# Performance work log

Measured on AMD Instinct MI355X. Metric: run time of the kernel, lower is better.

Reference implementation:

```python
import jax, jax.numpy as jnp
from jax import lax
import numpy as np

B = 8192
NUM_CTX = 300; NUM_STN = 300; NUM_GPE = 20; NUM_GPI = 2; NUM_OUT = 20
FF_DIM = 20; FF_STEPS = 20; STN_ITERS = 50
ETA_GPE = 1.0; ETA_STN = 1.0 / 3.0; ETA_GPI = 0.1
A1 = 1.0; A2 = 1.0; THETAD1 = 0.0; THETAD2 = 0.0
UNITS = (64, 128, 64)

_SPECS = [("vf0", UNITS[0], NUM_CTX), ("vf1", UNITS[1], UNITS[0]), ("vf2", UNITS[2], UNITS[1]), ("vf3", 1, UNITS[2]),
          ("jd1", FF_DIM, NUM_CTX), ("jd2", FF_DIM, NUM_CTX), ("kd1", FF_DIM, NUM_CTX), ("kd2", FF_DIM, NUM_CTX),
          ("sg", NUM_GPE, NUM_STN), ("gs", NUM_STN, NUM_GPE), ("glat", NUM_GPE, NUM_GPE), ("slat", NUM_STN, NUM_STN),
          ("d1gpi", NUM_GPI, FF_DIM), ("stngpi", NUM_GPI, NUM_STN),
          ("ih", 4 * NUM_OUT, NUM_GPI), ("hh", 4 * NUM_OUT, NUM_OUT)]


def _lin_init(k, out_d, in_d):
    kw, kb = jax.random.split(k)
    bound = 1.0 / np.sqrt(in_d)
    w = jax.random.uniform(kw, (out_d, in_d), minval=-bound, maxval=bound, dtype=jnp.float32)
    b = jax.random.uniform(kb, (out_d,), minval=-bound, maxval=bound, dtype=jnp.float32)
    return w, b


def setup_inputs() -> dict:
    key = jax.random.key(0)
    ks = iter(jax.random.split(key, 40))
    inp = {}
    inp["stimulus"] = jax.random.normal(next(ks), (B, NUM_CTX), dtype=jnp.float32)
    inp["deltavf"] = jax.random.normal(next(ks), (B, 1), dtype=jnp.float32)
    inp["hx0"] = jax.random.uniform(next(ks), (B, NUM_OUT), dtype=jnp.float32)
    inp["cx0"] = jax.random.uniform(next(ks), (B, NUM_OUT), dtype=jnp.float32)
    for name, o, i in _SPECS:
        w, b = _lin_init(next(ks), o, i)
        inp["w_" + name] = w
        inp["b_" + name] = b
    return inp


def _lin(x, w, b):
    return x @ w.T + b


def _lstm_cell(x, h, c, w_ih, b_ih, w_hh, b_hh):
    gates = _lin(x, w_ih, b_ih) + _lin(h, w_hh, b_hh)
    i, f, g, o = jnp.split(gates, 4, axis=-1)  # torch LSTMCell gate order
    c_new = jax.nn.sigmoid(f) * c + jax.nn.sigmoid(i) * jnp.tanh(g)
    h_new = jax.nn.sigmoid(o) * jnp.tanh(c_new)
    return h_new, c_new


def reference(stimulus, deltavf, hx0, cx0,
              w_vf0, b_vf0, w_vf1, b_vf1, w_vf2, b_vf2, w_vf3, b_vf3,
              w_jd1, b_jd1, w_jd2, b_jd2, w_kd1, b_kd1, w_kd2, b_kd2,
              w_sg, b_sg, w_gs, b_gs, w_glat, b_glat, w_slat, b_slat,
              w_d1gpi, b_d1gpi, w_stngpi, b_stngpi,
              w_ih, b_ih, w_hh, b_hh):
    bsz = stimulus.shape[0]
    # value function head
    h = jax.nn.relu(_lin(stimulus, w_vf0, b_vf0))
    h = jax.nn.relu(_lin(h, w_vf1, b_vf1))
    h = jax.nn.relu(_lin(h, w_vf2, b_vf2))
    vt = jnp.tanh(_lin(h, w_vf3, b_vf3))  # [B, 1]

    lamd1 = jax.nn.sigmoid(A1 * (deltavf - THETAD1))  # [B, 1]
    lamd2 = jax.nn.sigmoid(A2 * (deltavf - THETAD2))  # [B, 1]

    # loop-invariant striatal drives (computed every iter in torch, same value)
    J_D1 = _lin(stimulus, w_jd1, b_jd1)
    J_D2 = _lin(stimulus, w_jd2, b_jd2)
    K_D1 = _lin(stimulus, w_kd1, b_kd1)
    K_D2 = _lin(stimulus, w_kd2, b_kd2)

    def ff_step(carry, _):
        v1, v2 = carry
        v1 = jax.nn.sigmoid(lamd1 * (J_D1 * (1.0 - v1) + (1.0 - K_D1) * v1))
        v2 = jax.nn.sigmoid(lamd2 * (J_D2 * (1.0 - v2) + (1.0 - K_D2) * v2))
        return (v1, v2), None

    z_ff = jnp.zeros((bsz, FF_DIM), dtype=stimulus.dtype)
    (V_D1, V_D2), _ = lax.scan(ff_step, (z_ff, z_ff), None, length=FF_STEPS)

    V_GPi_DP = _lin(V_D1, w_d1gpi, b_d1gpi)  # [B, num_gpi]

    def stn_step(carry, _):
        xgpe, xstn, vstn, vgpi, hx, cx = carry
        xgpe = xgpe + ETA_GPE * (-xgpe + _lin(vstn, w_sg, b_sg) + _lin(xgpe, w_glat, b_glat) - V_D2)
        xstn = xstn + ETA_STN * (-xstn + _lin(xgpe, w_gs, b_gs) + _lin(vstn, w_slat, b_slat))
        vstn = jnp.tanh(lamd2 * xstn)
        V_GPi_IP = lamd2 * _lin(vstn, w_stngpi, b_stngpi)
        vgpi = vgpi + ETA_GPI * (-vgpi - V_GPi_DP + 2.0 * V_GPi_IP)
        hx, cx = _lstm_cell(-vgpi, hx, cx, w_ih, b_ih, w_hh, b_hh)
        return (xgpe, xstn, vstn, vgpi, hx, cx), None

    carry0 = (jnp.zeros((bsz, NUM_GPE), dtype=stimulus.dtype),
              jnp.zeros((bsz, NUM_STN), dtype=stimulus.dtype),
              jnp.zeros((bsz, NUM_STN), dtype=stimulus.dtype),  # tanh(lamd2*0) = 0
              jnp.zeros((bsz, NUM_GPI), dtype=stimulus.dtype),
              hx0, cx0)
    carry, _ = lax.scan(stn_step, carry0, None, length=STN_ITERS)
    hx = carry[4]
    return hx, vt
```

## Files before the change

kernel.cpp:

```cpp
#include <hip/hip_runtime.h>


typedef _Float16 f16_t;
typedef _Float16 f16x8 __attribute__((ext_vector_type(8)));
typedef _Float16 f16x4 __attribute__((ext_vector_type(4)));
typedef float floatx4 __attribute__((ext_vector_type(4)));
typedef float floatx2 __attribute__((ext_vector_type(2)));

#define BTOT 8192
#define BM   32
#define NTHR 512
#define NBLK 256
#define VSTR 328
#define XST  32

struct Params {
  const float *stimulus, *deltavf, *hx0, *cx0;
  const float *w_vf0, *b_vf0, *w_vf1, *b_vf1, *w_vf2, *b_vf2, *w_vf3, *b_vf3;
  const float *w_jd1, *b_jd1, *w_jd2, *b_jd2, *w_kd1, *b_kd1, *w_kd2, *b_kd2;
  const float *w_sg, *b_sg, *w_gs, *b_gs, *w_glat, *b_glat, *w_slat, *b_slat;
  const float *w_d1gpi, *b_d1gpi, *w_stngpi, *b_stngpi;
  const float *w_ih, *b_ih, *w_hh, *b_hh;
  float* out;
};

struct __align__(16) Smem {
  f16_t vstn[BM * VSTR];
  f16_t xgpe[2][BM * XST];
  f16_t hxf[BM * XST];
  f16_t wB2[21 * 512];
  f16_t wsp[10 * 512];
  f16_t whh[5 * 512];
  union { float h1f[BM * 128]; float scr[3200]; float gates[BM * 80]; } u;
  float h0f[BM * 64];
  float V_D2f[BM * 20];
  float lstmc[20][12];
  float bsumS[304];
  float bsg[20];
  float DPs[BM * 2], vgpis[BM * 2], lamS[BM];
};

__device__ __forceinline__ float rcp_f(float x) { return __builtin_amdgcn_rcpf(x); }
__device__ __forceinline__ float sigm_fast(float x) { return rcp_f(1.f + __expf(-x)); }
__device__ __forceinline__ float tanh_fast(float x) { return 1.f - 2.f * rcp_f(1.f + __expf(2.f * x)); }

__device__ __forceinline__ f16x8 ldfrag(const float* row, int k0, int kmax, bool valid) {
  float4 z = make_float4(0.f, 0.f, 0.f, 0.f);
  int nv = valid ? (kmax - k0) : 0;
  float4 f0 = (nv >= 4) ? *(const float4*)(row + k0) : z;
  float4 f1 = (nv >= 8) ? *(const float4*)(row + k0 + 4) : z;
  f16x8 r;
  r[0] = (f16_t)f0.x; r[1] = (f16_t)f0.y; r[2] = (f16_t)f0.z; r[3] = (f16_t)f0.w;
  r[4] = (f16_t)f1.x; r[5] = (f16_t)f1.y; r[6] = (f16_t)f1.z; r[7] = (f16_t)f1.w;
  return r;
}

__global__ __launch_bounds__(NTHR, 2) void bg_main(Params P) {
  __shared__ Smem S;
  const int tid  = threadIdx.x;
  const int lane = tid & 63;
  const int wv   = tid >> 6;
  const int q    = lane >> 4;
  const int cl   = lane & 15;
  const int row0 = blockIdx.x * BM;
  const floatx4 zf = {0.f, 0.f, 0.f, 0.f};

  if (tid < BM) S.lamS[tid] = sigm_fast(P.deltavf[row0 + tid]);
  for (int i = tid; i < BM * 2; i += NTHR) S.vgpis[i] = 0.f;
  for (int i = tid; i < 2 * BM * XST; i += NTHR) ((f16_t*)S.xgpe)[i] = (f16_t)0.f;
  for (int i = tid; i < BM * XST; i += NTHR) {
    int m = i >> 5, j = i & 31;
    S.hxf[i] = (j < 20) ? (f16_t)P.hx0[row0 * 20 + m * 20 + j] : (f16_t)0.f;
  }
  for (int i = tid; i < BM * VSTR; i += NTHR) S.vstn[i] = (f16_t)0.f;
  for (int i = tid; i < 21 * 512; i += NTHR) {
    int t = i >> 9, l = (i >> 3) & 63, jj = i & 7;
    int c2 = l & 15, k = ((l >> 4) << 3) + jj;
    float v = 0.f;
    if (t < 19) { int n = t * 16 + c2; if (n < 300 && k < 20) v = P.w_gs[n * 20 + k]; }
    else        { int g = (t - 19) * 16 + c2; if (g < 20 && k < 20) v = P.w_glat[g * 20 + k]; }
    S.wB2[i] = (f16_t)v;
  }
  for (int i = tid; i < 10 * 512; i += NTHR) {
    int c = i >> 9, l = (i >> 3) & 63, jj = i & 7;
    int p = l & 15, k = c * 32 + ((l >> 4) << 3) + jj;
    float v = (p < 2 && k < 300) ? P.w_stngpi[p * 300 + k] : 0.f;
    S.wsp[i] = (f16_t)v;
  }
  for (int i = tid; i < 5 * 512; i += NTHR) {
    int t = i >> 9, l = (i >> 3) & 63, jj = i & 7;
    int c2 = l & 15, k = ((l >> 4) << 3) + jj;
    int orig = (c2 & 3) * 20 + 4 * t + (c2 >> 2);
    S.whh[i] = (f16_t)((k < 20) ? P.w_hh[orig * 20 + k] : 0.f);
  }
  for (int i = tid; i < 240; i += NTHR) {
    int j = i / 12, c = i - j * 12;
    float v;
    if (c < 4)      v = P.b_ih[c * 20 + j] + P.b_hh[c * 20 + j];
    else if (c < 8) v = P.w_ih[((c - 4) * 20 + j) * 2 + 0];
    else            v = P.w_ih[((c - 8) * 20 + j) * 2 + 1];
    S.lstmc[j][c] = v;
  }
  for (int i = tid; i < 304; i += NTHR) S.bsumS[i] = (i < 300) ? (P.b_slat[i] + P.b_gs[i]) : 0.f;
  for (int i = tid; i < 20; i += NTHR)  S.bsg[i] = P.b_sg[i] + P.b_glat[i];

  {
    int o = tid & 63, mb = (tid >> 6) * 4;
    const float4* wr = (const float4*)(P.w_vf0 + o * 300);
    float bias = P.b_vf0[o], a[4];
#pragma unroll
    for (int u = 0; u < 4; ++u) a[u] = bias;
    for (int kq = 0; kq < 75; ++kq) {
      float4 w = wr[kq];
#pragma unroll
      for (int u = 0; u < 4; ++u) {
        float4 v = *(const float4*)(P.stimulus + (size_t)(row0 + mb + u) * 300 + kq * 4);
        a[u] = fmaf(v.x, w.x, a[u]); a[u] = fmaf(v.y, w.y, a[u]);
        a[u] = fmaf(v.z, w.z, a[u]); a[u] = fmaf(v.w, w.w, a[u]);
      }
    }
#pragma unroll
    for (int u = 0; u < 4; ++u) S.h0f[(mb + u) * 64 + o] = fmaxf(a[u], 0.f);
  }
  __syncthreads();
  {
    int o = tid & 127, mb = (tid >> 7) * 8;
    const float* wr = P.w_vf1 + o * 64;
    float bias = P.b_vf1[o], a[8];
#pragma unroll
    for (int u = 0; u < 8; ++u) a[u] = bias;
    for (int k = 0; k < 64; ++k) {
      float w = wr[k];
#pragma unroll
      for (int u = 0; u < 8; ++u) a[u] = fmaf(S.h0f[(mb + u) * 64 + k], w, a[u]);
    }
#pragma unroll
    for (int u = 0; u < 8; ++u) S.u.h1f[(mb + u) * 128 + o] = fmaxf(a[u], 0.f);
  }
  __syncthreads();
  {
    int o = tid & 63, mb = (tid >> 6) * 4;
    const float* wr = P.w_vf2 + o * 128;
    float bias = P.b_vf2[o], a[4];
#pragma unroll
    for (int u = 0; u < 4; ++u) a[u] = bias;
    for (int k = 0; k < 128; ++k) {
      float w = wr[k];
#pragma unroll
      for (int u = 0; u < 4; ++u) a[u] = fmaf(S.u.h1f[(mb + u) * 128 + k], w, a[u]);
    }
#pragma unroll
    for (int u = 0; u < 4; ++u) S.h0f[(mb + u) * 64 + o] = fmaxf(a[u], 0.f);
  }
  __syncthreads();
  {
    int oid = tid & 127, mb = (tid >> 7) * 8;
    if (oid < 80) {
      int which = oid / 20, o = oid - which * 20;
      const float *wp, *bp;
      if (which == 0)      { wp = P.w_jd1; bp = P.b_jd1; }
      else if (which == 1) { wp = P.w_jd2; bp = P.b_jd2; }
      else if (which == 2) { wp = P.w_kd1; bp = P.b_kd1; }
      else                 { wp = P.w_kd2; bp = P.b_kd2; }
      float bias = bp[o], a[8];
#pragma unroll
      for (int u = 0; u < 8; ++u) a[u] = bias;
      for (int kq = 0; kq < 75; ++kq) {
        float4 w = *(const float4*)(wp + o * 300 + kq * 4);
#pragma unroll
        for (int u = 0; u < 8; ++u) {
          float4 v = *(const float4*)(P.stimulus + (size_t)(row0 + mb + u) * 300 + kq * 4);
          a[u] = fmaf(v.x, w.x, a[u]); a[u] = fmaf(v.y, w.y, a[u]);
          a[u] = fmaf(v.z, w.z, a[u]); a[u] = fmaf(v.w, w.w, a[u]);
        }
      }
#pragma unroll
      for (int u = 0; u < 8; ++u) S.u.scr[which * 640 + (mb + u) * 20 + o] = a[u];
    }
    if (tid < BM) {
      float a = P.b_vf3[0];
      for (int k = 0; k < 64; ++k) a = fmaf(S.h0f[tid * 64 + k], P.w_vf3[k], a);
      P.out[(size_t)BTOT * 20 + row0 + tid] = tanh_fast(a);
    }
  }
  __syncthreads();
  for (int i = tid; i < BM * 20; i += NTHR) {
    int m = i / 20;
    float j1 = S.u.scr[i],        j2 = S.u.scr[640 + i];
    float k1 = S.u.scr[1280 + i], k2 = S.u.scr[1920 + i];
    float L = S.lamS[m], v1 = 0.f, v2 = 0.f;
    for (int s = 0; s < 20; ++s) {
      v1 = sigm_fast(L * (j1 * (1.f - v1) + (1.f - k1) * v1));
      v2 = sigm_fast(L * (j2 * (1.f - v2) + (1.f - k2) * v2));
    }
    S.u.scr[2560 + i] = v1;
    S.V_D2f[i] = v2;
  }
  __syncthreads();
  if (tid < BM * 2) {
    int m = tid >> 1, p2 = tid & 1;
    float a = P.b_d1gpi[p2];
    for (int o = 0; o < 20; ++o) a = fmaf(S.u.scr[2560 + m * 20 + o], P.w_d1gpi[p2 * 20 + o], a);
    S.DPs[tid] = a;
  }
  __syncthreads();

  f16x8 Ws[3][10];
#pragma unroll
  for (int j = 0; j < 3; ++j) {
    int t = wv + 8 * j;
    if (t < 19) {
      int n = t * 16 + cl;
#pragma unroll
      for (int c = 0; c < 10; ++c)
        Ws[j][c] = ldfrag(P.w_slat + (size_t)(n < 300 ? n : 0) * 300, c * 32 + q * 8, 300, n < 300);
    } else if (t < 21) {
      int g = (t - 19) * 16 + cl;
#pragma unroll
      for (int c = 0; c < 10; ++c)
        Ws[j][c] = ldfrag(P.w_sg + (size_t)(g < 20 ? g : 0) * 300, c * 32 + q * 8, 300, g < 20);
    } else {
      f16x8 z;
#pragma unroll
      for (int e = 0; e < 8; ++e) z[e] = (f16_t)0.f;
#pragma unroll
      for (int c = 0; c < 10; ++c) Ws[j][c] = z;
    }
  }
  const float lam0 = S.lamS[cl], lam1 = S.lamS[cl + 16];
  const float bstn0 = P.b_stngpi[0], bstn1 = P.b_stngpi[1];
  const int e0 = tid,        m0 = e0 / 20, j0 = e0 - m0 * 20;
  const int e1 = tid + NTHR, m1 = e1 / 20, j1 = e1 - m1 * 20;
  const bool hase1 = (tid < BM * 20 - NTHR);
  float cxr0 = P.cx0[row0 * 20 + e0], hxr0 = P.hx0[row0 * 20 + e0];
  float cxr1 = hase1 ? P.cx0[row0 * 20 + e1] : 0.f;
  float hxr1 = hase1 ? P.hx0[row0 * 20 + e1] : 0.f;
  const bool isSgW = (wv == 3 || wv == 4);

  floatx4 acc[3][2];
#pragma unroll
  for (int j = 0; j < 3; ++j) { acc[j][0] = zf; acc[j][1] = zf; }

  for (int it = 0; it < 50; ++it) {
    const int po = it & 1, pn = po ^ 1;
    if (isSgW) { acc[2][0] = zf; acc[2][1] = zf; }

    __builtin_amdgcn_s_setprio(1);
#pragma unroll
    for (int c = 0; c < 10; ++c) {
      f16x8 b0 = *(const f16x8*)&S.vstn[cl * VSTR + c * 32 + q * 8];
      f16x8 b1 = *(const f16x8*)&S.vstn[(16 + cl) * VSTR + c * 32 + q * 8];
#pragma unroll
      for (int j = 0; j < 3; ++j) {
        if (wv + 8 * j < 21) {
          acc[j][0] = __builtin_amdgcn_mfma_f32_16x16x32_f16(Ws[j][c], b0, acc[j][0], 0, 0, 0);
          acc[j][1] = __builtin_amdgcn_mfma_f32_16x16x32_f16(Ws[j][c], b1, acc[j][1], 0, 0, 0);
        }
      }
    }
    __builtin_amdgcn_s_setprio(0);
    if (isSgW) {
      f16x8 Wg = *(const f16x8*)&S.wB2[(wv + 16) * 512 + lane * 8];
      f16x8 g0 = *(const f16x8*)&S.xgpe[po][cl * XST + q * 8];
      f16x8 g1 = *(const f16x8*)&S.xgpe[po][(16 + cl) * XST + q * 8];
      acc[2][0] = __builtin_amdgcn_mfma_f32_16x16x32_f16(Wg, g0, acc[2][0], 0, 0, 0);
      acc[2][1] = __builtin_amdgcn_mfma_f32_16x16x32_f16(Wg, g1, acc[2][1], 0, 0, 0);
      int g0i = (wv - 3) * 16 + q * 4;
      if (g0i < 20) {
        floatx4 bg4 = *(const floatx4*)&S.bsg[g0i];
#pragma unroll
        for (int mf = 0; mf < 2; ++mf) {
          int batch = cl + 16 * mf;
          floatx4 vd4 = *(const floatx4*)&S.V_D2f[batch * 20 + g0i];
          f16x4 pk;
#pragma unroll
          for (int r = 0; r < 4; ++r) pk[r] = (f16_t)(acc[2][mf][r] + bg4[r] - vd4[r]);
          *(f16x4*)&S.xgpe[pn][batch * XST + g0i] = pk;
        }
      }
    }
    __syncthreads();

    {
      f16x8 x0 = *(const f16x8*)&S.xgpe[pn][cl * XST + q * 8];
      f16x8 x1 = *(const f16x8*)&S.xgpe[pn][(16 + cl) * XST + q * 8];
      if (wv < 5) {
        f16x8 Wh = *(const f16x8*)&S.whh[wv * 512 + lane * 8];
        f16x8 h0 = *(const f16x8*)&S.hxf[cl * XST + q * 8];
        f16x8 h1 = *(const f16x8*)&S.hxf[(16 + cl) * XST + q * 8];
        floatx4 gA = __builtin_amdgcn_mfma_f32_16x16x32_f16(Wh, h0, zf, 0, 0, 0);
        floatx4 gB = __builtin_amdgcn_mfma_f32_16x16x32_f16(Wh, h1, zf, 0, 0, 0);
        int gb = wv * 16 + q * 4;
        *(floatx4*)&S.u.gates[cl * 80 + gb] = gA;
        *(floatx4*)&S.u.gates[(cl + 16) * 80 + gb] = gB;
      }
#pragma unroll
      for (int j = 0; j < 3; ++j) {
        int t = wv + 8 * j;
        if (t < 19) {
          f16x8 Wg = *(const f16x8*)&S.wB2[t * 512 + lane * 8];
          acc[j][0] = __builtin_amdgcn_mfma_f32_16x16x32_f16(Wg, x0, acc[j][0], 0, 0, 0);
          acc[j][1] = __builtin_amdgcn_mfma_f32_16x16x32_f16(Wg, x1, acc[j][1], 0, 0, 0);
        }
      }
#pragma unroll
      for (int j = 0; j < 3; ++j) {
        int t = wv + 8 * j;
        if (t < 19) {
          int n0 = t * 16 + q * 4;
          if (!(t == 18 && q == 3)) {
            floatx4 bs4 = *(const floatx4*)&S.bsumS[n0];
#pragma unroll
            for (int mf = 0; mf < 2; ++mf) {
              float lm = mf ? lam1 : lam0;
              f16x4 pk;
#pragma unroll
              for (int r = 0; r < 4; ++r) {
                float tmp = acc[j][mf][r] + bs4[r];
                float xn  = tmp * (1.0f / 3.0f);
                acc[j][mf][r] = tmp * (2.0f / 3.0f);
                pk[r] = (f16_t)tanh_fast(lm * xn);
              }
              *(f16x4*)&S.vstn[(cl + 16 * mf) * VSTR + n0] = pk;
            }
          }
        }
      }
    }
    __syncthreads();

    if (wv == 5) {
      floatx4 ip0 = zf, ip1 = zf;
#pragma unroll
      for (int c = 0; c < 10; ++c) {
        f16x8 Wp = *(const f16x8*)&S.wsp[c * 512 + lane * 8];
        f16x8 b0 = *(const f16x8*)&S.vstn[cl * VSTR + c * 32 + q * 8];
        f16x8 b1 = *(const f16x8*)&S.vstn[(16 + cl) * VSTR + c * 32 + q * 8];
        ip0 = __builtin_amdgcn_mfma_f32_16x16x32_f16(Wp, b0, ip0, 0, 0, 0);
        ip1 = __builtin_amdgcn_mfma_f32_16x16x32_f16(Wp, b1, ip1, 0, 0, 0);
      }
      if (q == 0) {
#pragma unroll
        for (int mf = 0; mf < 2; ++mf) {
          int batch = cl + 16 * mf;
          float lm = mf ? lam1 : lam0;
          floatx2 vg = *(const floatx2*)&S.vgpis[batch * 2];
          floatx2 dp = *(const floatx2*)&S.DPs[batch * 2];
          float ipa = lm * ((mf ? ip1[0] : ip0[0]) + bstn0);
          float ipb = lm * ((mf ? ip1[1] : ip0[1]) + bstn1);
          vg[0] = vg[0] + 0.1f * (-vg[0] - dp[0] + 2.f * ipa);
          vg[1] = vg[1] + 0.1f * (-vg[1] - dp[1] + 2.f * ipb);
          *(floatx2*)&S.vgpis[batch * 2] = vg;
        }
      }
    }
    __syncthreads();

    {
      floatx4 g4 = *(const floatx4*)&S.u.gates[m0 * 80 + j0 * 4];
      floatx4 cb = *(const floatx4*)&S.lstmc[j0][0];
      floatx4 w0 = *(const floatx4*)&S.lstmc[j0][4];
      floatx4 w1 = *(const floatx4*)&S.lstmc[j0][8];
      floatx2 vg = *(const floatx2*)&S.vgpis[m0 * 2];
      float gi = g4[0] + cb[0] - w0[0] * vg[0] - w1[0] * vg[1];
      float gf = g4[1] + cb[1] - w0[1] * vg[0] - w1[1] * vg[1];
      float gg = g4[2] + cb[2] - w0[2] * vg[0] - w1[2] * vg[1];
      float go = g4[3] + cb[3] - w0[3] * vg[0] - w1[3] * vg[1];
      float cn = sigm_fast(gf) * cxr0 + sigm_fast(gi) * tanh_fast(gg);
      cxr0 = cn;
      hxr0 = sigm_fast(go) * tanh_fast(cn);
      S.hxf[m0 * XST + j0] = (f16_t)hxr0;
    }
    if (hase1) {
      floatx4 g4 = *(const floatx4*)&S.u.gates[m1 * 80 + j1 * 4];
      floatx4 cb = *(const floatx4*)&S.lstmc[j1][0];
      floatx4 w0 = *(const floatx4*)&S.lstmc[j1][4];
      floatx4 w1 = *(const floatx4*)&S.lstmc[j1][8];
      floatx2 vg = *(const floatx2*)&S.vgpis[m1 * 2];
      float gi = g4[0] + cb[0] - w0[0] * vg[0] - w1[0] * vg[1];
      float gf = g4[1] + cb[1] - w0[1] * vg[0] - w1[1] * vg[1];
      float gg = g4[2] + cb[2] - w0[2] * vg[0] - w1[2] * vg[1];
      float go = g4[3] + cb[3] - w0[3] * vg[0] - w1[3] * vg[1];
      float cn = sigm_fast(gf) * cxr1 + sigm_fast(gi) * tanh_fast(gg);
      cxr1 = cn;
      hxr1 = sigm_fast(go) * tanh_fast(cn);
      S.hxf[m1 * XST + j1] = (f16_t)hxr1;
    }
  }

  P.out[(size_t)row0 * 20 + e0] = hxr0;
  if (hase1) P.out[(size_t)row0 * 20 + e1] = hxr1;
}

extern "C" void kernel_launch(void* const* d_in, const int* in_sizes, int n_in,
                              void* d_out, int out_size, void* d_ws, size_t ws_size,
                              hipStream_t stream) {
  (void)in_sizes; (void)n_in; (void)out_size; (void)d_ws; (void)ws_size;
  Params P;
  P.stimulus = (const float*)d_in[0];
  P.deltavf  = (const float*)d_in[1];
  P.hx0 = (const float*)d_in[2];
  P.cx0 = (const float*)d_in[3];
  P.w_vf0 = (const float*)d_in[4];  P.b_vf0 = (const float*)d_in[5];
  P.w_vf1 = (const float*)d_in[6];  P.b_vf1 = (const float*)d_in[7];
  P.w_vf2 = (const float*)d_in[8];  P.b_vf2 = (const float*)d_in[9];
  P.w_vf3 = (const float*)d_in[10]; P.b_vf3 = (const float*)d_in[11];
  P.w_jd1 = (const float*)d_in[12]; P.b_jd1 = (const float*)d_in[13];
  P.w_jd2 = (const float*)d_in[14]; P.b_jd2 = (const float*)d_in[15];
  P.w_kd1 = (const float*)d_in[16]; P.b_kd1 = (const float*)d_in[17];
  P.w_kd2 = (const float*)d_in[18]; P.b_kd2 = (const float*)d_in[19];
  P.w_sg  = (const float*)d_in[20]; P.b_sg  = (const float*)d_in[21];
  P.w_gs  = (const float*)d_in[22]; P.b_gs  = (const float*)d_in[23];
  P.w_glat= (const float*)d_in[24]; P.b_glat= (const float*)d_in[25];
  P.w_slat= (const float*)d_in[26]; P.b_slat= (const float*)d_in[27];
  P.w_d1gpi  = (const float*)d_in[28]; P.b_d1gpi  = (const float*)d_in[29];
  P.w_stngpi = (const float*)d_in[30]; P.b_stngpi = (const float*)d_in[31];
  P.w_ih = (const float*)d_in[32]; P.b_ih = (const float*)d_in[33];
  P.w_hh = (const float*)d_in[34]; P.b_hh = (const float*)d_in[35];
  P.out  = (float*)d_out;
  bg_main<<<NBLK, NTHR, 0, stream>>>(P);
}
```

Before: 408.2 us.

## Double threads per block and redistribute STN recurrence tiles across sixteen waves

Raises the block to 1024 threads with one block per CU and redistributes the 21 MFMA output tiles of the STN/GPe recurrence so each of 16 waves owns at most two tiles. The second tile's weights now come from a new shared-memory staging buffer instead of registers. The LSTM gate MFMAs, the GPi reduction and the elementwise LSTM update move to otherwise idle waves, so the update runs in one pass per element. The aim is shorter per-iteration critical paths and lower register pressure, at the cost of more LDS, lower block occupancy and extra LDS reads each iteration.

```diff
diff --git a/kernel.cpp b/kernel.cpp
--- a/kernel.cpp
+++ b/kernel.cpp
@@ -9,7 +9,7 @@
 
 #define BTOT 8192
 #define BM   32
-#define NTHR 512
+#define NTHR 1024
 #define NBLK 256
 #define VSTR 328
 #define XST  32
@@ -29,6 +29,7 @@
   f16_t xgpe[2][BM * XST];
   f16_t hxf[BM * XST];
   f16_t wB2[21 * 512];
+  f16_t ws1[5 * 10 * 512];
   f16_t wsp[10 * 512];
   f16_t whh[5 * 512];
   union { float h1f[BM * 128]; float scr[3200]; float gates[BM * 80]; } u;
@@ -55,7 +56,7 @@
   return r;
 }
 
-__global__ __launch_bounds__(NTHR, 2) void bg_main(Params P) {
+__global__ __launch_bounds__(NTHR, 1) void bg_main(Params P) {
   __shared__ Smem S;
   const int tid  = threadIdx.x;
   const int lane = tid & 63;
@@ -65,12 +66,16 @@
   const int row0 = blockIdx.x * BM;
   const floatx4 zf = {0.f, 0.f, 0.f, 0.f};
 
+  const bool has1  = (wv < 5);
+  const bool isSgW = (wv == 3 || wv == 4);
+  const int  gtile = (wv >= 5 && wv < 10) ? (wv - 5) : -1;
+
   if (tid < BM) S.lamS[tid] = sigm_fast(P.deltavf[row0 + tid]);
   for (int i = tid; i < BM * 2; i += NTHR) S.vgpis[i] = 0.f;
   for (int i = tid; i < 2 * BM * XST; i += NTHR) ((f16_t*)S.xgpe)[i] = (f16_t)0.f;
   for (int i = tid; i < BM * XST; i += NTHR) {
     int m = i >> 5, j = i & 31;
-    S.hxf[i] = (j < 20) ? (f16_t)P.hx0[row0 * 20 + m * 20 + j] : (f16_t)0.f;
+    S.hxf[i] = (j < 20) ? (f16_t)P.hx0[(size_t)(row0 + m) * 20 + j] : (f16_t)0.f;
   }
   for (int i = tid; i < BM * VSTR; i += NTHR) S.vstn[i] = (f16_t)0.f;
   for (int i = tid; i < 21 * 512; i += NTHR) {
@@ -81,6 +86,16 @@
     else        { int g = (t - 19) * 16 + c2; if (g < 20 && k < 20) v = P.w_glat[g * 20 + k]; }
     S.wB2[i] = (f16_t)v;
   }
+  for (int i = tid; i < 5 * 5120; i += NTHR) {
+    int t5 = i / 5120, rem = i - t5 * 5120;
+    int c = rem >> 9, l = (rem >> 3) & 63, jj = i & 7;
+    int c2 = l & 15, k = c * 32 + ((l >> 4) << 3) + jj;
+    int t = 16 + t5;
+    float v = 0.f;
+    if (t < 19) { int n = t * 16 + c2; if (n < 300 && k < 300) v = P.w_slat[(size_t)n * 300 + k]; }
+    else        { int g = (t - 19) * 16 + c2; if (g < 20 && k < 300) v = P.w_sg[(size_t)g * 300 + k]; }
+    S.ws1[i] = (f16_t)v;
+  }
   for (int i = tid; i < 10 * 512; i += NTHR) {
     int c = i >> 9, l = (i >> 3) & 63, jj = i & 7;
     int p = l & 15, k = c * 32 + ((l >> 4) << 3) + jj;
@@ -105,56 +120,54 @@
   for (int i = tid; i < 20; i += NTHR)  S.bsg[i] = P.b_sg[i] + P.b_glat[i];
 
   {
-    int o = tid & 63, mb = (tid >> 6) * 4;
+    int o = tid & 63, mb = (tid >> 6) * 2;
     const float4* wr = (const float4*)(P.w_vf0 + o * 300);
-    float bias = P.b_vf0[o], a[4];
-#pragma unroll
-    for (int u = 0; u < 4; ++u) a[u] = bias;
+    float bias = P.b_vf0[o], a[2];
+    a[0] = bias; a[1] = bias;
     for (int kq = 0; kq < 75; ++kq) {
       float4 w = wr[kq];
 #pragma unroll
-      for (int u = 0; u < 4; ++u) {
+      for (int u = 0; u < 2; ++u) {
         float4 v = *(const float4*)(P.stimulus + (size_t)(row0 + mb + u) * 300 + kq * 4);
         a[u] = fmaf(v.x, w.x, a[u]); a[u] = fmaf(v.y, w.y, a[u]);
         a[u] = fmaf(v.z, w.z, a[u]); a[u] = fmaf(v.w, w.w, a[u]);
       }
     }
 #pragma unroll
-    for (int u = 0; u < 4; ++u) S.h0f[(mb + u) * 64 + o] = fmaxf(a[u], 0.f);
+    for (int u = 0; u < 2; ++u) S.h0f[(mb + u) * 64 + o] = fmaxf(a[u], 0.f);
   }
   __syncthreads();
   {
-    int o = tid & 127, mb = (tid >> 7) * 8;
+    int o = tid & 127, mb = (tid >> 7) * 4;
     const float* wr = P.w_vf1 + o * 64;
-    float bias = P.b_vf1[o], a[8];
-#pragma unroll
-    for (int u = 0; u < 8; ++u) a[u] = bias;
+    float bias = P.b_vf1[o], a[4];
+#pragma unroll
+    for (int u = 0; u < 4; ++u) a[u] = bias;
     for (int k = 0; k < 64; ++k) {
       float w = wr[k];
 #pragma unroll
-      for (int u = 0; u < 8; ++u) a[u] = fmaf(S.h0f[(mb + u) * 64 + k], w, a[u]);
-    }
-#pragma unroll
-    for (int u = 0; u < 8; ++u) S.u.h1f[(mb + u) * 128 + o] = fmaxf(a[u], 0.f);
+      for (int u = 0; u < 4; ++u) a[u] = fmaf(S.h0f[(mb + u) * 64 + k], w, a[u]);
+    }
+#pragma unroll
+    for (int u = 0; u < 4; ++u) S.u.h1f[(mb + u) * 128 + o] = fmaxf(a[u], 0.f);
   }
   __syncthreads();
   {
-    int o = tid & 63, mb = (tid >> 6) * 4;
+    int o = tid & 63, mb = (tid >> 6) * 2;
     const float* wr = P.w_vf2 + o * 128;
-    float bias = P.b_vf2[o], a[4];
-#pragma unroll
-    for (int u = 0; u < 4; ++u) a[u] = bias;
+    float bias = P.b_vf2[o], a[2];
+    a[0] = bias; a[1] = bias;
     for (int k = 0; k < 128; ++k) {
       float w = wr[k];
 #pragma unroll
-      for (int u = 0; u < 4; ++u) a[u] = fmaf(S.u.h1f[(mb + u) * 128 + k], w, a[u]);
-    }
-#pragma unroll
-    for (int u = 0; u < 4; ++u) S.h0f[(mb + u) * 64 + o] = fmaxf(a[u], 0.f);
+      for (int u = 0; u < 2; ++u) a[u] = fmaf(S.u.h1f[(mb + u) * 128 + k], w, a[u]);
+    }
+#pragma unroll
+    for (int u = 0; u < 2; ++u) S.h0f[(mb + u) * 64 + o] = fmaxf(a[u], 0.f);
   }
   __syncthreads();
   {
-    int oid = tid & 127, mb = (tid >> 7) * 8;
+    int oid = tid & 127, mb = (tid >> 7) * 4;
     if (oid < 80) {
       int which = oid / 20, o = oid - which * 20;
       const float *wp, *bp;
@@ -162,20 +175,20 @@
       else if (which == 1) { wp = P.w_jd2; bp = P.b_jd2; }
       else if (which == 2) { wp = P.w_kd1; bp = P.b_kd1; }
       else                 { wp = P.w_kd2; bp = P.b_kd2; }
-      float bias = bp[o], a[8];
-#pragma unroll
-      for (int u = 0; u < 8; ++u) a[u] = bias;
+      float bias = bp[o], a[4];
+#pragma unroll
+      for (int u = 0; u < 4; ++u) a[u] = bias;
       for (int kq = 0; kq < 75; ++kq) {
         float4 w = *(const float4*)(wp + o * 300 + kq * 4);
 #pragma unroll
-        for (int u = 0; u < 8; ++u) {
+        for (int u = 0; u < 4; ++u) {
           float4 v = *(const float4*)(P.stimulus + (size_t)(row0 + mb + u) * 300 + kq * 4);
           a[u] = fmaf(v.x, w.x, a[u]); a[u] = fmaf(v.y, w.y, a[u]);
           a[u] = fmaf(v.z, w.z, a[u]); a[u] = fmaf(v.w, w.w, a[u]);
         }
       }
 #pragma unroll
-      for (int u = 0; u < 8; ++u) S.u.scr[which * 640 + (mb + u) * 20 + o] = a[u];
+      for (int u = 0; u < 4; ++u) S.u.scr[which * 640 + (mb + u) * 20 + o] = a[u];
     }
     if (tid < BM) {
       float a = P.b_vf3[0];
@@ -205,66 +218,56 @@
   }
   __syncthreads();
 
-  f16x8 Ws[3][10];
-#pragma unroll
-  for (int j = 0; j < 3; ++j) {
-    int t = wv + 8 * j;
-    if (t < 19) {
-      int n = t * 16 + cl;
-#pragma unroll
-      for (int c = 0; c < 10; ++c)
-        Ws[j][c] = ldfrag(P.w_slat + (size_t)(n < 300 ? n : 0) * 300, c * 32 + q * 8, 300, n < 300);
-    } else if (t < 21) {
-      int g = (t - 19) * 16 + cl;
-#pragma unroll
-      for (int c = 0; c < 10; ++c)
-        Ws[j][c] = ldfrag(P.w_sg + (size_t)(g < 20 ? g : 0) * 300, c * 32 + q * 8, 300, g < 20);
-    } else {
-      f16x8 z;
-#pragma unroll
-      for (int e = 0; e < 8; ++e) z[e] = (f16_t)0.f;
-#pragma unroll
-      for (int c = 0; c < 10; ++c) Ws[j][c] = z;
-    }
+  f16x8 Ws0[10];
+  {
+    int n = wv * 16 + cl;
+    const float* a0 = P.w_slat + (size_t)n * 300;
+#pragma unroll
+    for (int c = 0; c < 10; ++c) Ws0[c] = ldfrag(a0, c * 32 + q * 8, 300, true);
   }
   const float lam0 = S.lamS[cl], lam1 = S.lamS[cl + 16];
   const float bstn0 = P.b_stngpi[0], bstn1 = P.b_stngpi[1];
-  const int e0 = tid,        m0 = e0 / 20, j0 = e0 - m0 * 20;
-  const int e1 = tid + NTHR, m1 = e1 / 20, j1 = e1 - m1 * 20;
-  const bool hase1 = (tid < BM * 20 - NTHR);
-  float cxr0 = P.cx0[row0 * 20 + e0], hxr0 = P.hx0[row0 * 20 + e0];
-  float cxr1 = hase1 ? P.cx0[row0 * 20 + e1] : 0.f;
-  float hxr1 = hase1 ? P.hx0[row0 * 20 + e1] : 0.f;
-  const bool isSgW = (wv == 3 || wv == 4);
-
-  floatx4 acc[3][2];
-#pragma unroll
-  for (int j = 0; j < 3; ++j) { acc[j][0] = zf; acc[j][1] = zf; }
+  const bool lown = (tid >= 384);
+  const int  e0 = lown ? (tid - 384) : 0;
+  const int  m0 = e0 / 20, j0 = e0 - m0 * 20;
+  float cxr0 = lown ? P.cx0[(size_t)row0 * 20 + e0] : 0.f;
+  float hxr0 = 0.f;
+
+  floatx4 acc[2][2];
+  acc[0][0] = zf; acc[0][1] = zf; acc[1][0] = zf; acc[1][1] = zf;
 
   for (int it = 0; it < 50; ++it) {
     const int po = it & 1, pn = po ^ 1;
-    if (isSgW) { acc[2][0] = zf; acc[2][1] = zf; }
+    if (isSgW) { acc[1][0] = zf; acc[1][1] = zf; }
 
     __builtin_amdgcn_s_setprio(1);
-#pragma unroll
-    for (int c = 0; c < 10; ++c) {
-      f16x8 b0 = *(const f16x8*)&S.vstn[cl * VSTR + c * 32 + q * 8];
-      f16x8 b1 = *(const f16x8*)&S.vstn[(16 + cl) * VSTR + c * 32 + q * 8];
-#pragma unroll
-      for (int j = 0; j < 3; ++j) {
-        if (wv + 8 * j < 21) {
-          acc[j][0] = __builtin_amdgcn_mfma_f32_16x16x32_f16(Ws[j][c], b0, acc[j][0], 0, 0, 0);
-          acc[j][1] = __builtin_amdgcn_mfma_f32_16x16x32_f16(Ws[j][c], b1, acc[j][1], 0, 0, 0);
-        }
+    if (has1) {
+#pragma unroll
+      for (int c = 0; c < 10; ++c) {
+        f16x8 b0 = *(const f16x8*)&S.vstn[cl * VSTR + c * 32 + q * 8];
+        f16x8 b1 = *(const f16x8*)&S.vstn[(16 + cl) * VSTR + c * 32 + q * 8];
+        f16x8 a1 = *(const f16x8*)&S.ws1[(wv * 10 + c) * 512 + lane * 8];
+        acc[0][0] = __builtin_amdgcn_mfma_f32_16x16x32_f16(Ws0[c], b0, acc[0][0], 0, 0, 0);
+        acc[0][1] = __builtin_amdgcn_mfma_f32_16x16x32_f16(Ws0[c], b1, acc[0][1], 0, 0, 0);
+        acc[1][0] = __builtin_amdgcn_mfma_f32_16x16x32_f16(a1, b0, acc[1][0], 0, 0, 0);
+        acc[1][1] = __builtin_amdgcn_mfma_f32_16x16x32_f16(a1, b1, acc[1][1], 0, 0, 0);
+      }
+    } else {
+#pragma unroll
+      for (int c = 0; c < 10; ++c) {
+        f16x8 b0 = *(const f16x8*)&S.vstn[cl * VSTR + c * 32 + q * 8];
+        f16x8 b1 = *(const f16x8*)&S.vstn[(16 + cl) * VSTR + c * 32 + q * 8];
+        acc[0][0] = __builtin_amdgcn_mfma_f32_16x16x32_f16(Ws0[c], b0, acc[0][0], 0, 0, 0);
+        acc[0][1] = __builtin_amdgcn_mfma_f32_16x16x32_f16(Ws0[c], b1, acc[0][1], 0, 0, 0);
       }
     }
     __builtin_amdgcn_s_setprio(0);
     if (isSgW) {
-      f16x8 Wg = *(const f16x8*)&S.wB2[(wv + 16) * 512 + lane * 8];
+      f16x8 Wg = *(const f16x8*)&S.wB2[(16 + wv) * 512 + lane * 8];
       f16x8 g0 = *(const f16x8*)&S.xgpe[po][cl * XST + q * 8];
       f16x8 g1 = *(const f16x8*)&S.xgpe[po][(16 + cl) * XST + q * 8];
-      acc[2][0] = __builtin_amdgcn_mfma_f32_16x16x32_f16(Wg, g0, acc[2][0], 0, 0, 0);
-      acc[2][1] = __builtin_amdgcn_mfma_f32_16x16x32_f16(Wg, g1, acc[2][1], 0, 0, 0);
+      acc[1][0] = __builtin_amdgcn_mfma_f32_16x16x32_f16(Wg, g0, acc[1][0], 0, 0, 0);
+      acc[1][1] = __builtin_amdgcn_mfma_f32_16x16x32_f16(Wg, g1, acc[1][1], 0, 0, 0);
       int g0i = (wv - 3) * 16 + q * 4;
       if (g0i < 20) {
         floatx4 bg4 = *(const floatx4*)&S.bsg[g0i];
@@ -274,7 +277,7 @@
           floatx4 vd4 = *(const floatx4*)&S.V_D2f[batch * 20 + g0i];
           f16x4 pk;
 #pragma unroll
-          for (int r = 0; r < 4; ++r) pk[r] = (f16_t)(acc[2][mf][r] + bg4[r] - vd4[r]);
+          for (int r = 0; r < 4; ++r) pk[r] = (f16_t)(acc[1][mf][r] + bg4[r] - vd4[r]);
           *(f16x4*)&S.xgpe[pn][batch * XST + g0i] = pk;
         }
       }
@@ -284,19 +287,19 @@
     {
       f16x8 x0 = *(const f16x8*)&S.xgpe[pn][cl * XST + q * 8];
       f16x8 x1 = *(const f16x8*)&S.xgpe[pn][(16 + cl) * XST + q * 8];
-      if (wv < 5) {
-        f16x8 Wh = *(const f16x8*)&S.whh[wv * 512 + lane * 8];
+      if (gtile >= 0) {
+        f16x8 Wh = *(const f16x8*)&S.whh[gtile * 512 + lane * 8];
         f16x8 h0 = *(const f16x8*)&S.hxf[cl * XST + q * 8];
         f16x8 h1 = *(const f16x8*)&S.hxf[(16 + cl) * XST + q * 8];
         floatx4 gA = __builtin_amdgcn_mfma_f32_16x16x32_f16(Wh, h0, zf, 0, 0, 0);
         floatx4 gB = __builtin_amdgcn_mfma_f32_16x16x32_f16(Wh, h1, zf, 0, 0, 0);
-        int gb = wv * 16 + q * 4;
+        int gb = gtile * 16 + q * 4;
         *(floatx4*)&S.u.gates[cl * 80 + gb] = gA;
         *(floatx4*)&S.u.gates[(cl + 16) * 80 + gb] = gB;
       }
 #pragma unroll
-      for (int j = 0; j < 3; ++j) {
-        int t = wv + 8 * j;
+      for (int j = 0; j < 2; ++j) {
+        int t = j ? (has1 ? 16 + wv : 99) : wv;
         if (t < 19) {
           f16x8 Wg = *(const f16x8*)&S.wB2[t * 512 + lane * 8];
           acc[j][0] = __builtin_amdgcn_mfma_f32_16x16x32_f16(Wg, x0, acc[j][0], 0, 0, 0);
@@ -304,8 +307,8 @@
         }
       }
 #pragma unroll
-      for (int j = 0; j < 3; ++j) {
-        int t = wv + 8 * j;
+      for (int j = 0; j < 2; ++j) {
+        int t = j ? (has1 ? 16 + wv : 99) : wv;
         if (t < 19) {
           int n0 = t * 16 + q * 4;
           if (!(t == 18 && q == 3)) {
@@ -329,7 +332,7 @@
     }
     __syncthreads();
 
-    if (wv == 5) {
+    if (wv == 10) {
       floatx4 ip0 = zf, ip1 = zf;
 #pragma unroll
       for (int c = 0; c < 10; ++c) {
@@ -356,7 +359,7 @@
     }
     __syncthreads();
 
-    {
+    if (lown) {
       floatx4 g4 = *(const floatx4*)&S.u.gates[m0 * 80 + j0 * 4];
       floatx4 cb = *(const floatx4*)&S.lstmc[j0][0];
       floatx4 w0 = *(const floatx4*)&S.lstmc[j0][4];
@@ -371,25 +374,9 @@
       hxr0 = sigm_fast(go) * tanh_fast(cn);
       S.hxf[m0 * XST + j0] = (f16_t)hxr0;
     }
-    if (hase1) {
-      floatx4 g4 = *(const floatx4*)&S.u.gates[m1 * 80 + j1 * 4];
-      floatx4 cb = *(const floatx4*)&S.lstmc[j1][0];
-      floatx4 w0 = *(const floatx4*)&S.lstmc[j1][4];
-      floatx4 w1 = *(const floatx4*)&S.lstmc[j1][8];
-      floatx2 vg = *(const floatx2*)&S.vgpis[m1 * 2];
-      float gi = g4[0] + cb[0] - w0[0] * vg[0] - w1[0] * vg[1];
-      float gf = g4[1] + cb[1] - w0[1] * vg[0] - w1[1] * vg[1];
-      float gg = g4[2] + cb[2] - w0[2] * vg[0] - w1[2] * vg[1];
-      float go = g4[3] + cb[3] - w0[3] * vg[0] - w1[3] * vg[1];
-      float cn = sigm_fast(gf) * cxr1 + sigm_fast(gi) * tanh_fast(gg);
-      cxr1 = cn;
-      hxr1 = sigm_fast(go) * tanh_fast(cn);
-      S.hxf[m1 * XST + j1] = (f16_t)hxr1;
-    }
-  }
-
-  P.out[(size_t)row0 * 20 + e0] = hxr0;
-  if (hase1) P.out[(size_t)row0 * 20 + e1] = hxr1;
+  }
+
+  if (lown) P.out[(size_t)row0 * 20 + e0] = hxr0;
 }
 
 extern "C" void kernel_launch(void* const* d_in, const int* in_sizes, int n_in,
```

New measurement: 411.1 us. Within noise of the previous version (+0.7%).

## Fuse STN-to-GPi projection into vstn epilogue and drop a barrier

Applied to the files above, without the earlier changes.

The STN-to-GPi dot product, previously a separate single-wave MFMA pass behind its own barrier, is now computed in fp32 inside the vstn tanh epilogue. Partials are reduced with lane shuffles and written to a small per-wave buffer. The LSTM threads sum the eight wave partials and keep the vgpi state in registers, which removes one __syncthreads per iteration and the serialized wave-5 phase. Separately, the two GPe waves now compute their GPe rows first so the xgpe write is issued before their remaining STN MFMAs. The cost is extra FMAs and shuffles in every wave's epilogue plus redundant partial summation in the LSTM step.

```diff
diff --git a/kernel.cpp b/kernel.cpp
--- a/kernel.cpp
+++ b/kernel.cpp
@@ -29,15 +29,16 @@
   f16_t xgpe[2][BM * XST];
   f16_t hxf[BM * XST];
   f16_t wB2[21 * 512];
-  f16_t wsp[10 * 512];
   f16_t whh[5 * 512];
   union { float h1f[BM * 128]; float scr[3200]; float gates[BM * 80]; } u;
   float h0f[BM * 64];
   float V_D2f[BM * 20];
   float lstmc[20][12];
+  float wspf[2][304];
+  float pp[8][64];
   float bsumS[304];
   float bsg[20];
-  float DPs[BM * 2], vgpis[BM * 2], lamS[BM];
+  float DPs[BM * 2], lamS[BM];
 };
 
 __device__ __forceinline__ float rcp_f(float x) { return __builtin_amdgcn_rcpf(x); }
@@ -66,7 +67,6 @@
   const floatx4 zf = {0.f, 0.f, 0.f, 0.f};
 
   if (tid < BM) S.lamS[tid] = sigm_fast(P.deltavf[row0 + tid]);
-  for (int i = tid; i < BM * 2; i += NTHR) S.vgpis[i] = 0.f;
   for (int i = tid; i < 2 * BM * XST; i += NTHR) ((f16_t*)S.xgpe)[i] = (f16_t)0.f;
   for (int i = tid; i < BM * XST; i += NTHR) {
     int m = i >> 5, j = i & 31;
@@ -81,17 +81,15 @@
     else        { int g = (t - 19) * 16 + c2; if (g < 20 && k < 20) v = P.w_glat[g * 20 + k]; }
     S.wB2[i] = (f16_t)v;
   }
-  for (int i = tid; i < 10 * 512; i += NTHR) {
-    int c = i >> 9, l = (i >> 3) & 63, jj = i & 7;
-    int p = l & 15, k = c * 32 + ((l >> 4) << 3) + jj;
-    float v = (p < 2 && k < 300) ? P.w_stngpi[p * 300 + k] : 0.f;
-    S.wsp[i] = (f16_t)v;
-  }
   for (int i = tid; i < 5 * 512; i += NTHR) {
     int t = i >> 9, l = (i >> 3) & 63, jj = i & 7;
     int c2 = l & 15, k = ((l >> 4) << 3) + jj;
     int orig = (c2 & 3) * 20 + 4 * t + (c2 >> 2);
     S.whh[i] = (f16_t)((k < 20) ? P.w_hh[orig * 20 + k] : 0.f);
+  }
+  for (int i = tid; i < 2 * 304; i += NTHR) {
+    int p = i / 304, k = i - p * 304;
+    S.wspf[p][k] = (k < 300) ? P.w_stngpi[p * 300 + k] : 0.f;
   }
   for (int i = tid; i < 240; i += NTHR) {
     int j = i / 12, c = i - j * 12;
@@ -235,6 +233,7 @@
   float cxr0 = P.cx0[row0 * 20 + e0], hxr0 = P.hx0[row0 * 20 + e0];
   float cxr1 = hase1 ? P.cx0[row0 * 20 + e1] : 0.f;
   float hxr1 = hase1 ? P.hx0[row0 * 20 + e1] : 0.f;
+  float vgA0 = 0.f, vgA1 = 0.f, vgB0 = 0.f, vgB1 = 0.f;
   const bool isSgW = (wv == 3 || wv == 4);
 
   floatx4 acc[3][2];
@@ -243,44 +242,64 @@
 
   for (int it = 0; it < 50; ++it) {
     const int po = it & 1, pn = po ^ 1;
-    if (isSgW) { acc[2][0] = zf; acc[2][1] = zf; }
 
     __builtin_amdgcn_s_setprio(1);
-#pragma unroll
-    for (int c = 0; c < 10; ++c) {
-      f16x8 b0 = *(const f16x8*)&S.vstn[cl * VSTR + c * 32 + q * 8];
-      f16x8 b1 = *(const f16x8*)&S.vstn[(16 + cl) * VSTR + c * 32 + q * 8];
-#pragma unroll
-      for (int j = 0; j < 3; ++j) {
-        if (wv + 8 * j < 21) {
-          acc[j][0] = __builtin_amdgcn_mfma_f32_16x16x32_f16(Ws[j][c], b0, acc[j][0], 0, 0, 0);
-          acc[j][1] = __builtin_amdgcn_mfma_f32_16x16x32_f16(Ws[j][c], b1, acc[j][1], 0, 0, 0);
+    if (isSgW) {
+      acc[2][0] = zf; acc[2][1] = zf;
+#pragma unroll
+      for (int c = 0; c < 10; ++c) {
+        f16x8 b0 = *(const f16x8*)&S.vstn[cl * VSTR + c * 32 + q * 8];
+        f16x8 b1 = *(const f16x8*)&S.vstn[(16 + cl) * VSTR + c * 32 + q * 8];
+        acc[2][0] = __builtin_amdgcn_mfma_f32_16x16x32_f16(Ws[2][c], b0, acc[2][0], 0, 0, 0);
+        acc[2][1] = __builtin_amdgcn_mfma_f32_16x16x32_f16(Ws[2][c], b1, acc[2][1], 0, 0, 0);
+      }
+      {
+        f16x8 Wg = *(const f16x8*)&S.wB2[(wv + 16) * 512 + lane * 8];
+        f16x8 g0 = *(const f16x8*)&S.xgpe[po][cl * XST + q * 8];
+        f16x8 g1 = *(const f16x8*)&S.xgpe[po][(16 + cl) * XST + q * 8];
+        acc[2][0] = __builtin_amdgcn_mfma_f32_16x16x32_f16(Wg, g0, acc[2][0], 0, 0, 0);
+        acc[2][1] = __builtin_amdgcn_mfma_f32_16x16x32_f16(Wg, g1, acc[2][1], 0, 0, 0);
+        int g0i = (wv - 3) * 16 + q * 4;
+        if (g0i < 20) {
+          floatx4 bg4 = *(const floatx4*)&S.bsg[g0i];
+#pragma unroll
+          for (int mf = 0; mf < 2; ++mf) {
+            int batch = cl + 16 * mf;
+            floatx4 vd4 = *(const floatx4*)&S.V_D2f[batch * 20 + g0i];
+            f16x4 pk;
+#pragma unroll
+            for (int r = 0; r < 4; ++r) pk[r] = (f16_t)(acc[2][mf][r] + bg4[r] - vd4[r]);
+            *(f16x4*)&S.xgpe[pn][batch * XST + g0i] = pk;
+          }
         }
       }
+#pragma unroll
+      for (int c = 0; c < 10; ++c) {
+        f16x8 b0 = *(const f16x8*)&S.vstn[cl * VSTR + c * 32 + q * 8];
+        f16x8 b1 = *(const f16x8*)&S.vstn[(16 + cl) * VSTR + c * 32 + q * 8];
+        acc[0][0] = __builtin_amdgcn_mfma_f32_16x16x32_f16(Ws[0][c], b0, acc[0][0], 0, 0, 0);
+        acc[0][1] = __builtin_amdgcn_mfma_f32_16x16x32_f16(Ws[0][c], b1, acc[0][1], 0, 0, 0);
+        acc[1][0] = __builtin_amdgcn_mfma_f32_16x16x32_f16(Ws[1][c], b0, acc[1][0], 0, 0, 0);
+        acc[1][1] = __builtin_amdgcn_mfma_f32_16x16x32_f16(Ws[1][c], b1, acc[1][1], 0, 0, 0);
+      }
+    } else {
+#pragma unroll
+      for (int c = 0; c < 10; ++c) {
+        f16x8 b0 = *(const f16x8*)&S.vstn[cl * VSTR + c * 32 + q * 8];
+        f16x8 b1 = *(const f16x8*)&S.vstn[(16 + cl) * VSTR + c * 32 + q * 8];
+#pragma unroll
+        for (int j = 0; j < 3; ++j) {
+          if (wv + 8 * j < 21) {
+            acc[j][0] = __builtin_amdgcn_mfma_f32_16x16x32_f16(Ws[j][c], b0, acc[j][0], 0, 0, 0);
+            acc[j][1] = __builtin_amdgcn_mfma_f32_16x16x32_f16(Ws[j][c], b1, acc[j][1], 0, 0, 0);
+          }
+        }
+      }
     }
     __builtin_amdgcn_s_setprio(0);
-    if (isSgW) {
-      f16x8 Wg = *(const f16x8*)&S.wB2[(wv + 16) * 512 + lane * 8];
-      f16x8 g0 = *(const f16x8*)&S.xgpe[po][cl * XST + q * 8];
-      f16x8 g1 = *(const f16x8*)&S.xgpe[po][(16 + cl) * XST + q * 8];
-      acc[2][0] = __builtin_amdgcn_mfma_f32_16x16x32_f16(Wg, g0, acc[2][0], 0, 0, 0);
-      acc[2][1] = __builtin_amdgcn_mfma_f32_16x16x32_f16(Wg, g1, acc[2][1], 0, 0, 0);
-      int g0i = (wv - 3) * 16 + q * 4;
-      if (g0i < 20) {
-        floatx4 bg4 = *(const floatx4*)&S.bsg[g0i];
-#pragma unroll
-        for (int mf = 0; mf < 2; ++mf) {
-          int batch = cl + 16 * mf;
-          floatx4 vd4 = *(const floatx4*)&S.V_D2f[batch * 20 + g0i];
-          f16x4 pk;
-#pragma unroll
-          for (int r = 0; r < 4; ++r) pk[r] = (f16_t)(acc[2][mf][r] + bg4[r] - vd4[r]);
-          *(f16x4*)&S.xgpe[pn][batch * XST + g0i] = pk;
-        }
-      }
-    }
     __syncthreads();
 
+    float sp00 = 0.f, sp01 = 0.f, sp10 = 0.f, sp11 = 0.f;
     {
       f16x8 x0 = *(const f16x8*)&S.xgpe[pn][cl * XST + q * 8];
       f16x8 x1 = *(const f16x8*)&S.xgpe[pn][(16 + cl) * XST + q * 8];
@@ -310,6 +329,8 @@
           int n0 = t * 16 + q * 4;
           if (!(t == 18 && q == 3)) {
             floatx4 bs4 = *(const floatx4*)&S.bsumS[n0];
+            floatx4 w0 = *(const floatx4*)&S.wspf[0][n0];
+            floatx4 w1 = *(const floatx4*)&S.wspf[1][n0];
 #pragma unroll
             for (int mf = 0; mf < 2; ++mf) {
               float lm = mf ? lam1 : lam0;
@@ -319,68 +340,76 @@
                 float tmp = acc[j][mf][r] + bs4[r];
                 float xn  = tmp * (1.0f / 3.0f);
                 acc[j][mf][r] = tmp * (2.0f / 3.0f);
-                pk[r] = (f16_t)tanh_fast(lm * xn);
+                float vv = tanh_fast(lm * xn);
+                pk[r] = (f16_t)vv;
+                if (mf) { sp01 = fmaf(w0[r], vv, sp01); sp11 = fmaf(w1[r], vv, sp11); }
+                else    { sp00 = fmaf(w0[r], vv, sp00); sp10 = fmaf(w1[r], vv, sp10); }
               }
               *(f16x4*)&S.vstn[(cl + 16 * mf) * VSTR + n0] = pk;
             }
           }
         }
       }
+      sp00 += __shfl_xor(sp00, 16); sp00 += __shfl_xor(sp00, 32);
+      sp01 += __shfl_xor(sp01, 16); sp01 += __shfl_xor(sp01, 32);
+      sp10 += __shfl_xor(sp10, 16); sp10 += __shfl_xor(sp10, 32);
+      sp11 += __shfl_xor(sp11, 16); sp11 += __shfl_xor(sp11, 32);
+      if (q == 0) {
+        floatx2 a; a[0] = sp00; a[1] = sp10;
+        floatx2 b; b[0] = sp01; b[1] = sp11;
+        *(floatx2*)&S.pp[wv][cl * 2] = a;
+        *(floatx2*)&S.pp[wv][32 + cl * 2] = b;
+      }
     }
     __syncthreads();
 
-    if (wv == 5) {
-      floatx4 ip0 = zf, ip1 = zf;
-#pragma unroll
-      for (int c = 0; c < 10; ++c) {
-        f16x8 Wp = *(const f16x8*)&S.wsp[c * 512 + lane * 8];
-        f16x8 b0 = *(const f16x8*)&S.vstn[cl * VSTR + c * 32 + q * 8];
-        f16x8 b1 = *(const f16x8*)&S.vstn[(16 + cl) * VSTR + c * 32 + q * 8];
-        ip0 = __builtin_amdgcn_mfma_f32_16x16x32_f16(Wp, b0, ip0, 0, 0, 0);
-        ip1 = __builtin_amdgcn_mfma_f32_16x16x32_f16(Wp, b1, ip1, 0, 0, 0);
-      }
-      if (q == 0) {
-#pragma unroll
-        for (int mf = 0; mf < 2; ++mf) {
-          int batch = cl + 16 * mf;
-          float lm = mf ? lam1 : lam0;
-          floatx2 vg = *(const floatx2*)&S.vgpis[batch * 2];
-          floatx2 dp = *(const floatx2*)&S.DPs[batch * 2];
-          float ipa = lm * ((mf ? ip1[0] : ip0[0]) + bstn0);
-          float ipb = lm * ((mf ? ip1[1] : ip0[1]) + bstn1);
-          vg[0] = vg[0] + 0.1f * (-vg[0] - dp[0] + 2.f * ipa);
-          vg[1] = vg[1] + 0.1f * (-vg[1] - dp[1] + 2.f * ipb);
-          *(floatx2*)&S.vgpis[batch * 2] = vg;
-        }
-      }
-    }
-    __syncthreads();
-
     {
+      float sA = 0.f, sB = 0.f;
+#pragma unroll
+      for (int w = 0; w < 8; ++w) {
+        floatx2 t2 = *(const floatx2*)&S.pp[w][m0 * 2];
+        sA += t2[0]; sB += t2[1];
+      }
+      float lamr = S.lamS[m0];
+      floatx2 dp = *(const floatx2*)&S.DPs[m0 * 2];
+      float ipa = lamr * (sA + bstn0);
+      float ipb = lamr * (sB + bstn1);
+      vgA0 = vgA0 + 0.1f * (-vgA0 - dp[0] + 2.f * ipa);
+      vgA1 = vgA1 + 0.1f * (-vgA1 - dp[1] + 2.f * ipb);
       floatx4 g4 = *(const floatx4*)&S.u.gates[m0 * 80 + j0 * 4];
       floatx4 cb = *(const floatx4*)&S.lstmc[j0][0];
       floatx4 w0 = *(const floatx4*)&S.lstmc[j0][4];
       floatx4 w1 = *(const floatx4*)&S.lstmc[j0][8];
-      floatx2 vg = *(const floatx2*)&S.vgpis[m0 * 2];
-      float gi = g4[0] + cb[0] - w0[0] * vg[0] - w1[0] * vg[1];
-      float gf = g4[1] + cb[1] - w0[1] * vg[0] - w1[1] * vg[1];
-      float gg = g4[2] + cb[2] - w0[2] * vg[0] - w1[2] * vg[1];
-      float go = g4[3] + cb[3] - w0[3] * vg[0] - w1[3] * vg[1];
+      float gi = g4[0] + cb[0] - w0[0] * vgA0 - w1[0] * vgA1;
+      float gf = g4[1] + cb[1] - w0[1] * vgA0 - w1[1] * vgA1;
+      float gg = g4[2] + cb[2] - w0[2] * vgA0 - w1[2] * vgA1;
+      float go = g4[3] + cb[3] - w0[3] * vgA0 - w1[3] * vgA1;
       float cn = sigm_fast(gf) * cxr0 + sigm_fast(gi) * tanh_fast(gg);
       cxr0 = cn;
       hxr0 = sigm_fast(go) * tanh_fast(cn);
       S.hxf[m0 * XST + j0] = (f16_t)hxr0;
     }
     if (hase1) {
+      float sA = 0.f, sB = 0.f;
+#pragma unroll
+      for (int w = 0; w < 8; ++w) {
+        floatx2 t2 = *(const floatx2*)&S.pp[w][m1 * 2];
+        sA += t2[0]; sB += t2[1];
+      }
+      float lamr = S.lamS[m1];
+      floatx2 dp = *(const floatx2*)&S.DPs[m1 * 2];
+      float ipa = lamr * (sA + bstn0);
+      float ipb = lamr * (sB + bstn1);
+      vgB0 = vgB0 + 0.1f * (-vgB0 - dp[0] + 2.f * ipa);
+      vgB1 = vgB1 + 0.1f * (-vgB1 - dp[1] + 2.f * ipb);
       floatx4 g4 = *(const floatx4*)&S.u.gates[m1 * 80 + j1 * 4];
       floatx4 cb = *(const floatx4*)&S.lstmc[j1][0];
       floatx4 w0 = *(const floatx4*)&S.lstmc[j1][4];
       floatx4 w1 = *(const floatx4*)&S.lstmc[j1][8];
-      floatx2 vg = *(const floatx2*)&S.vgpis[m1 * 2];
-      float gi = g4[0] + cb[0] - w0[0] * vg[0] - w1[0] * vg[1];
-      float gf = g4[1] + cb[1] - w0[1] * vg[0] - w1[1] * vg[1];
-      float gg = g4[2] + cb[2] - w0[2] * vg[0] - w1[2] * vg[1];
-      float go = g4[3] + cb[3] - w0[3] * vg[0] - w1[3] * vg[1];
+      float gi = g4[0] + cb[0] - w0[0] * vgB0 - w1[0] * vgB1;
+      float gf = g4[1] + cb[1] - w0[1] * vgB0 - w1[1] * vgB1;
+      float gg = g4[2] + cb[2] - w0[2] * vgB0 - w1[2] * vgB1;
+      float go = g4[3] + cb[3] - w0[3] * vgB0 - w1[3] * vgB1;
       float cn = sigm_fast(gf) * cxr1 + sigm_fast(gi) * tanh_fast(gg);
       cxr1 = cn;
       hxr1 = sigm_fast(go) * tanh_fast(cn);
```

Result: slower. 455.6 us (+11.6%).
